# Optimization experiments

Hardware: AMD Instinct MI355X
Metric: run time of the kernel (lower is better)

The kernel has to match this reference:

```python
import jax, jax.numpy as jnp
import numpy as np

DIM = 256
NUM_HEADS = 4
HEAD_DIM = DIM // NUM_HEADS
MLP_HIDDEN = int(DIM * 2.0)
SCALE = HEAD_DIM ** -0.5
LN_EPS = 1e-5


def _layernorm(x, gamma, beta):
    mu = jnp.mean(x, axis=-1, keepdims=True)
    var = jnp.mean(jnp.square(x - mu), axis=-1, keepdims=True)
    return (x - mu) * jax.lax.rsqrt(var + LN_EPS) * gamma + beta


def setup_inputs() -> dict:
    key = jax.random.key(0)
    ks = jax.random.split(key, 8)
    B, C, N, P = 8, DIM, 64, 256
    s = 0.02
    return {
        "x": jax.random.normal(ks[0], (B, C, N, P), dtype=jnp.float32),
        # torch Linear weights stored [out_features, in_features]
        "W_qkv": jax.random.normal(ks[1], (3 * DIM, DIM), dtype=jnp.float32) * s,
        "W_proj": jax.random.normal(ks[2], (DIM, DIM), dtype=jnp.float32) * s,
        "b_proj": jnp.zeros((DIM,), dtype=jnp.float32),
        "ln1_g": jnp.ones((DIM,), dtype=jnp.float32),
        "ln1_b": jnp.zeros((DIM,), dtype=jnp.float32),
        "ln2_g": jnp.ones((DIM,), dtype=jnp.float32),
        "ln2_b": jnp.zeros((DIM,), dtype=jnp.float32),
        "W_mlp1": jax.random.normal(ks[3], (MLP_HIDDEN, DIM), dtype=jnp.float32) * s,
        "b_mlp1": jnp.zeros((MLP_HIDDEN,), dtype=jnp.float32),
        "W_mlp2": jax.random.normal(ks[4], (DIM, MLP_HIDDEN), dtype=jnp.float32) * s,
        "b_mlp2": jnp.zeros((DIM,), dtype=jnp.float32),
    }


def reference(x, W_qkv, W_proj, b_proj, ln1_g, ln1_b, ln2_g, ln2_b,
              W_mlp1, b_mlp1, W_mlp2, b_mlp2):
    B, C, N, P = x.shape
    H, D = NUM_HEADS, HEAD_DIM
    # [B,C,N,P] -> [B*N, P, C]
    x_seq = jnp.transpose(x, (0, 2, 3, 1)).reshape(B * N, P, C)
    shortcut = x_seq

    h = _layernorm(x_seq, ln1_g, ln1_b)
    qkv = jnp.einsum('spc,oc->spo', h, W_qkv)              # [BN, P, 3C]
    qkv = qkv.reshape(B * N, P, 3, H, D)
    q = jnp.transpose(qkv[:, :, 0], (0, 2, 1, 3))          # [BN, H, P, D]
    k = jnp.transpose(qkv[:, :, 1], (0, 2, 1, 3))
    v = jnp.transpose(qkv[:, :, 2], (0, 2, 1, 3))

    attn = jnp.einsum('shpd,shqd->shpq', q, k) * SCALE     # [BN, H, P, P]
    attn = jax.nn.softmax(attn, axis=-1)
    o = jnp.einsum('shpq,shqd->shpd', attn, v)             # [BN, H, P, D]
    o = jnp.transpose(o, (0, 2, 1, 3)).reshape(B * N, P, C)
    o = jnp.einsum('spc,oc->spo', o, W_proj) + b_proj

    x_seq = shortcut + o

    h2 = _layernorm(x_seq, ln2_g, ln2_b)
    m = jnp.einsum('spc,oc->spo', h2, W_mlp1) + b_mlp1
    m = jax.nn.gelu(m, approximate=False)
    m = jnp.einsum('sph,oh->spo', m, W_mlp2) + b_mlp2
    x_seq = x_seq + m

    out = x_seq.reshape(B, N, P, C)
    return jnp.transpose(out, (0, 3, 1, 2))                # [B, C, N, P]
```

## Files before the change

### kernel.cpp

```cpp
#include <hip/hip_runtime.h>
#include <stdint.h>
#include <math.h>


#define DEV static __device__ __forceinline__

typedef __bf16 bf16x8 __attribute__((ext_vector_type(8)));
typedef float  f32x4  __attribute__((ext_vector_type(4)));

union B8 { bf16x8 v; uint4 q; uint32_t u[4]; uint16_t h[8]; };

DEV uint16_t f2bf(float f) {
  uint32_t u = __float_as_uint(f);
  return (uint16_t)((u + 0x7FFFu + ((u >> 16) & 1u)) >> 16);
}
DEV float bf2f(uint16_t h) { return __uint_as_float(((uint32_t)h) << 16); }
DEV uint32_t pk2(float a, float b) { return (uint32_t)f2bf(a) | ((uint32_t)f2bf(b) << 16); }

DEV f32x4 mfma16(const B8& a, const B8& b, f32x4 c) {
  return __builtin_amdgcn_mfma_f32_16x16x32_bf16(a.v, b.v, c, 0, 0, 0);
}

DEV uint32_t shfl_u(uint32_t v, int src) { return (uint32_t)__shfl((int)v, src, 64); }

DEV B8 mk(const uint32_t* w) {
  B8 x; x.u[0] = w[0]; x.u[1] = w[1]; x.u[2] = w[2]; x.u[3] = w[3]; return x;
}

DEV void xpose(const uint32_t* pk0, const uint32_t* pk1, int kd, int g, int r, uint32_t* out) {
  const int sA = 32 * (g & 1) + r;
  const int sB = sA + 16;
  const int tA = 2 * kd, tB = 2 * kd + 1;
  uint32_t a0 = shfl_u(pk0[tA], sA), b0 = shfl_u(pk0[tB], sA);
  uint32_t a1 = shfl_u(pk1[tA], sA), b1 = shfl_u(pk1[tB], sA);
  uint32_t a2 = shfl_u(pk0[tA], sB), b2 = shfl_u(pk0[tB], sB);
  uint32_t a3 = shfl_u(pk1[tA], sB), b3 = shfl_u(pk1[tB], sB);
  const bool hi = g >= 2;
  out[0] = hi ? b0 : a0;
  out[1] = hi ? b1 : a1;
  out[2] = hi ? b2 : a2;
  out[3] = hi ? b3 : a3;
}

__global__ void transformer_prep(const float* __restrict__ wqkv,
                                 const float* __restrict__ wproj,
                                 const float* __restrict__ w1,
                                 const float* __restrict__ w2,
                                 uint16_t* __restrict__ dst) {
  int e = blockIdx.x * 256 + threadIdx.x;
  const float* src; int C, local;
  if (e < 196608)      { src = wqkv;  C = 256; local = e; }
  else if (e < 262144) { src = wproj; C = 256; local = e - 196608; }
  else if (e < 393216) { src = w1;    C = 256; local = e - 262144; }
  else                 { src = w2;    C = 512; local = e - 393216; }
  int k32 = C >> 5;
  int tile = local >> 9, within = local & 511;
  int ln = within >> 3, j = within & 7;
  int tr = tile / k32, tk = tile - tr * k32;
  int row = tr * 16 + (ln & 15), col = tk * 32 + (ln >> 4) * 8 + j;
  float v = src[row * C + col];
  if (e < 65536) v *= 0.18033688011112042f;
  dst[e] = f2bf(v);
}

__global__ __launch_bounds__(512, 2) void transformer_k1(
    const float* __restrict__ x,
    const float* __restrict__ bproj,
    const float* __restrict__ ln1g, const float* __restrict__ ln1b,
    const uint16_t* __restrict__ wf,
    uint16_t* __restrict__ osc,
    float* __restrict__ out) {
  __shared__ __attribute__((aligned(16))) uint8_t lds[65536];
  const int tid = threadIdx.x;
  const int lane = tid & 63;
  const int wv = tid >> 6;
  const int r = lane & 15;
  const int g = lane >> 4;
  const int s = blockIdx.x;
  const int bb = s >> 6, nn = s & 63;
  const float* xs = x + (size_t)bb * 4194304 + (size_t)nn * 256;
  float* outp = out + (size_t)bb * 4194304 + (size_t)nn * 256;
  const f32x4 fz = {0.f, 0.f, 0.f, 0.f};

  uint32_t hfrag[2][8][4];
  float s1[2] = {0.f, 0.f}, s2[2] = {0.f, 0.f};
#pragma unroll
  for (int rt = 0; rt < 2; ++rt) {
    int p = 32 * wv + 16 * rt + r;
#pragma unroll
    for (int kt = 0; kt < 8; ++kt) {
      int c0 = 32 * kt + 8 * g;
      float v[8];
#pragma unroll
      for (int j = 0; j < 8; ++j) {
        v[j] = xs[(size_t)(c0 + j) * 16384 + p];
        s1[rt] += v[j];
        s2[rt] += v[j] * v[j];
      }
#pragma unroll
      for (int w = 0; w < 4; ++w) hfrag[rt][kt][w] = pk2(v[2 * w], v[2 * w + 1]);
    }
  }
  float mu[2], rs[2];
#pragma unroll
  for (int rt = 0; rt < 2; ++rt) {
    float a = s1[rt]; a += __shfl_xor(a, 16, 64); a += __shfl_xor(a, 32, 64);
    float b = s2[rt]; b += __shfl_xor(b, 16, 64); b += __shfl_xor(b, 32, 64);
    mu[rt] = a * (1.0f / 256.0f);
    float var = b * (1.0f / 256.0f) - mu[rt] * mu[rt];
    rs[rt] = rsqrtf(var + 1e-5f);
  }
#pragma unroll
  for (int kt = 0; kt < 8; ++kt) {
    int c0 = 32 * kt + 8 * g;
    f32x4 gA = *(const f32x4*)(ln1g + c0), gB = *(const f32x4*)(ln1g + c0 + 4);
    f32x4 bA = *(const f32x4*)(ln1b + c0), bB = *(const f32x4*)(ln1b + c0 + 4);
#pragma unroll
    for (int rt = 0; rt < 2; ++rt) {
#pragma unroll
      for (int w = 0; w < 4; ++w) {
        uint32_t pw = hfrag[rt][kt][w];
        float lo = bf2f((uint16_t)(pw & 0xFFFFu));
        float hi = bf2f((uint16_t)(pw >> 16));
        float glo = (w < 2) ? gA[2 * w] : gB[2 * w - 4];
        float ghi = (w < 2) ? gA[2 * w + 1] : gB[2 * w - 3];
        float blo = (w < 2) ? bA[2 * w] : bB[2 * w - 4];
        float bhi = (w < 2) ? bA[2 * w + 1] : bB[2 * w - 3];
        lo = (lo - mu[rt]) * rs[rt] * glo + blo;
        hi = (hi - mu[rt]) * rs[rt] * ghi + bhi;
        hfrag[rt][kt][w] = pk2(lo, hi);
      }
    }
  }

#pragma unroll 1
  for (int hd = 0; hd < 4; ++hd) {
#pragma unroll
    for (int m = 0; m < 2; ++m) {
      f32x4 acc[2][4];
#pragma unroll
      for (int rt = 0; rt < 2; ++rt)
#pragma unroll
        for (int ct = 0; ct < 4; ++ct) acc[rt][ct] = fz;
#pragma unroll
      for (int kt = 0; kt < 8; ++kt) {
#pragma unroll
        for (int ct = 0; ct < 4; ++ct) {
          B8 wfr;
          wfr.q = *(const uint4*)(wf + (size_t)((((m + 1) * 16 + hd * 4 + ct) * 8 + kt) * 512) + lane * 8);
#pragma unroll
          for (int rt = 0; rt < 2; ++rt) {
            B8 a = mk(hfrag[rt][kt]);
            acc[rt][ct] = mfma16(a, wfr, acc[rt][ct]);
          }
        }
      }
#pragma unroll
      for (int rt = 0; rt < 2; ++rt) {
#pragma unroll
        for (int ct = 0; ct < 4; ++ct) {
          int d = 16 * ct + r;
          int q0 = 32 * wv + 16 * rt + 4 * g;
          if (m == 0) {
#pragma unroll
            for (int i = 0; i < 4; ++i) {
              int qq = q0 + i;
              *(uint16_t*)(lds + ((qq * 128 + d * 2) ^ ((qq & 7) << 4))) = f2bf(acc[rt][ct][i]);
            }
          } else {
            uint2 pv;
            pv.x = pk2(acc[rt][ct][0], acc[rt][ct][1]);
            pv.y = pk2(acc[rt][ct][2], acc[rt][ct][3]);
            *(uint2*)(lds + ((32768 + d * 512 + q0 * 2) ^ ((d & 7) << 4))) = pv;
          }
        }
      }
    }
    __syncthreads();

#pragma unroll 1
    for (int pt = 0; pt < 2; ++pt) {
      f32x4 qT[4];
#pragma unroll
      for (int mt = 0; mt < 4; ++mt) qT[mt] = fz;
#pragma unroll
      for (int kt = 0; kt < 8; ++kt) {
        B8 hb = mk(hfrag[pt][kt]);
#pragma unroll
        for (int mt = 0; mt < 4; ++mt) {
          B8 wa;
          wa.q = *(const uint4*)(wf + (size_t)(((hd * 4 + mt) * 8 + kt) * 512) + lane * 8);
          qT[mt] = mfma16(wa, hb, qT[mt]);
        }
      }
      uint32_t pq0[4], pq1[4];
#pragma unroll
      for (int mt = 0; mt < 4; ++mt) {
        pq0[mt] = pk2(qT[mt][0], qT[mt][1]);
        pq1[mt] = pk2(qT[mt][2], qT[mt][3]);
      }
      uint32_t qb[2][4];
#pragma unroll
      for (int kd = 0; kd < 2; ++kd) xpose(pq0, pq1, kd, g, r, qb[kd]);

      float m_ = -1e30f, l_ = 0.f;
      f32x4 oT[4];
#pragma unroll
      for (int dt = 0; dt < 4; ++dt) oT[dt] = fz;

#pragma unroll 1
      for (int chk = 0; chk < 4; ++chk) {
        f32x4 sT[4];
#pragma unroll
        for (int qt = 0; qt < 4; ++qt) sT[qt] = fz;
#pragma unroll
        for (int kd = 0; kd < 2; ++kd) {
          B8 qf = mk(qb[kd]);
#pragma unroll
          for (int qt = 0; qt < 4; ++qt) {
            int qq = chk * 64 + 16 * qt + r;
            B8 ka;
            ka.q = *(const uint4*)(lds + ((qq * 128 + (32 * kd + 8 * g) * 2) ^ ((qq & 7) << 4)));
            sT[qt] = mfma16(ka, qf, sT[qt]);
          }
        }
        float tmax = sT[0][0];
#pragma unroll
        for (int qt = 0; qt < 4; ++qt)
#pragma unroll
          for (int i = 0; i < 4; ++i) tmax = fmaxf(tmax, sT[qt][i]);
        tmax = fmaxf(tmax, __shfl_xor(tmax, 16, 64));
        tmax = fmaxf(tmax, __shfl_xor(tmax, 32, 64));
        float mn = fmaxf(m_, tmax);
        float fcor = exp2f(m_ - mn);
        float ts = 0.f;
#pragma unroll
        for (int qt = 0; qt < 4; ++qt)
#pragma unroll
          for (int i = 0; i < 4; ++i) {
            float e = exp2f(sT[qt][i] - mn);
            sT[qt][i] = e;
            ts += e;
          }
        ts += __shfl_xor(ts, 16, 64);
        ts += __shfl_xor(ts, 32, 64);
        l_ = l_ * fcor + ts;
        m_ = mn;
#pragma unroll
        for (int dt = 0; dt < 4; ++dt)
#pragma unroll
          for (int i = 0; i < 4; ++i) oT[dt][i] *= fcor;
        uint32_t pp0[4], pp1[4];
#pragma unroll
        for (int qt = 0; qt < 4; ++qt) {
          pp0[qt] = pk2(sT[qt][0], sT[qt][1]);
          pp1[qt] = pk2(sT[qt][2], sT[qt][3]);
        }
#pragma unroll
        for (int qk = 0; qk < 2; ++qk) {
          uint32_t pb[4];
          xpose(pp0, pp1, qk, g, r, pb);
          B8 pf = mk(pb);
#pragma unroll
          for (int dt = 0; dt < 4; ++dt) {
            B8 va;
            va.q = *(const uint4*)(lds + ((32768 + (16 * dt + r) * 512 + (chk * 64 + 32 * qk + 8 * g) * 2) ^ ((r & 7) << 4)));
            oT[dt] = mfma16(va, pf, oT[dt]);
          }
        }
      }
      float inv = 1.0f / l_;
      uint32_t po0[4], po1[4];
#pragma unroll
      for (int dt = 0; dt < 4; ++dt) {
        po0[dt] = pk2(oT[dt][0] * inv, oT[dt][1] * inv);
        po1[dt] = pk2(oT[dt][2] * inv, oT[dt][3] * inv);
      }
#pragma unroll
      for (int kd = 0; kd < 2; ++kd) {
        uint32_t ofr[4];
        xpose(po0, po1, kd, g, r, ofr);
        B8 t; t.u[0] = ofr[0]; t.u[1] = ofr[1]; t.u[2] = ofr[2]; t.u[3] = ofr[3];
        *(uint4*)(osc + (size_t)((s * 16 + 2 * wv + pt) * 8 + 2 * hd + kd) * 512 + lane * 8) = t.q;
      }
    }
    __syncthreads();
  }

#pragma unroll 1
  for (int q3 = 0; q3 < 4; ++q3) {
    f32x4 acc[2][4];
#pragma unroll
    for (int rt = 0; rt < 2; ++rt)
#pragma unroll
      for (int ct = 0; ct < 4; ++ct) acc[rt][ct] = fz;
#pragma unroll
    for (int kt = 0; kt < 8; ++kt) {
      B8 a[2];
#pragma unroll
      for (int rt = 0; rt < 2; ++rt)
        a[rt].q = *(const uint4*)(osc + (size_t)((s * 16 + 2 * wv + rt) * 8 + kt) * 512 + lane * 8);
#pragma unroll
      for (int ct = 0; ct < 4; ++ct) {
        B8 wfr;
        wfr.q = *(const uint4*)(wf + 196608 + (size_t)(((q3 * 4 + ct) * 8 + kt) * 512) + lane * 8);
#pragma unroll
        for (int rt = 0; rt < 2; ++rt) acc[rt][ct] = mfma16(a[rt], wfr, acc[rt][ct]);
      }
    }
#pragma unroll
    for (int rt = 0; rt < 2; ++rt) {
#pragma unroll
      for (int ct = 0; ct < 4; ++ct) {
        int c = q3 * 64 + 16 * ct + r;
        float bias = bproj[c];
        int p0 = 32 * wv + 16 * rt + 4 * g;
        f32x4 res = *(const f32x4*)(xs + (size_t)c * 16384 + p0);
        f32x4 x2v;
#pragma unroll
        for (int i = 0; i < 4; ++i) x2v[i] = acc[rt][ct][i] + bias + res[i];
        *(f32x4*)(outp + (size_t)c * 16384 + p0) = x2v;
      }
    }
  }
}

__global__ __launch_bounds__(512, 2) void transformer_k2(
    const float* __restrict__ ln2g, const float* __restrict__ ln2b,
    const uint16_t* __restrict__ w1f, const uint16_t* __restrict__ w2f,
    const float* __restrict__ bm1, const float* __restrict__ bm2,
    float* __restrict__ out) {
  __shared__ __attribute__((aligned(16))) uint8_t lds[68608];
  const int tid = threadIdx.x;
  const int lane = tid & 63;
  const int wv = tid >> 6;
  const int r = lane & 15, g = lane >> 4;
  const int bid = blockIdx.x;
  const int s = bid >> 2, tg = bid & 3;
  const int bb = s >> 6, nn = s & 63;
  float* outp = out + (size_t)bb * 4194304 + (size_t)nn * 256;
  const int tokbase = tg * 64;
  const f32x4 fz = {0.f, 0.f, 0.f, 0.f};
  const int mtw = wv & 3, kth = wv >> 2;
  const int p = tokbase + 16 * mtw + r;

  float v[4][8];
  float s1 = 0.f, s2 = 0.f;
#pragma unroll
  for (int k2l = 0; k2l < 4; ++k2l) {
    int c0 = (kth * 4 + k2l) * 32 + 8 * g;
#pragma unroll
    for (int j = 0; j < 8; ++j) {
      float t = outp[(size_t)(c0 + j) * 16384 + p];
      v[k2l][j] = t;
      s1 += t;
      s2 += t * t;
    }
  }
  s1 += __shfl_xor(s1, 16, 64); s1 += __shfl_xor(s1, 32, 64);
  s2 += __shfl_xor(s2, 16, 64); s2 += __shfl_xor(s2, 32, 64);
  if (g == 0) {
    float2 pr; pr.x = s1; pr.y = s2;
    *(float2*)(lds + 65536 + ((16 * mtw + r) * 2 + kth) * 8) = pr;
  }
  __syncthreads();
  if (tid < 64) {
    float2 a = *(const float2*)(lds + 65536 + (tid * 2 + 0) * 8);
    float2 b = *(const float2*)(lds + 65536 + (tid * 2 + 1) * 8);
    float su = a.x + b.x, sq = a.y + b.y;
    float m = su * (1.0f / 256.0f);
    float var = sq * (1.0f / 256.0f) - m * m;
    float2 st; st.x = m; st.y = rsqrtf(var + 1e-5f);
    *(float2*)(lds + 66560 + tid * 8) = st;
  }
  __syncthreads();
  float2 st = *(const float2*)(lds + 66560 + (16 * mtw + r) * 8);
#pragma unroll
  for (int k2l = 0; k2l < 4; ++k2l) {
    int kt = kth * 4 + k2l;
    int c0 = kt * 32 + 8 * g;
    f32x4 gA = *(const f32x4*)(ln2g + c0), gB = *(const f32x4*)(ln2g + c0 + 4);
    f32x4 bA = *(const f32x4*)(ln2b + c0), bB = *(const f32x4*)(ln2b + c0 + 4);
    float nv[8];
#pragma unroll
    for (int j = 0; j < 8; ++j) {
      float gg = (j < 4) ? gA[j] : gB[j - 4];
      float bb2 = (j < 4) ? bA[j] : bB[j - 4];
      nv[j] = (v[k2l][j] - st.x) * st.y * gg + bb2;
    }
    B8 t;
#pragma unroll
    for (int w = 0; w < 4; ++w) t.u[w] = pk2(nv[2 * w], nv[2 * w + 1]);
    *(uint4*)(lds + (mtw * 8 + kt) * 1024 + lane * 16) = t.q;
  }
  __syncthreads();

  f32x4 acc2[4][2];
#pragma unroll
  for (int mt = 0; mt < 4; ++mt)
#pragma unroll
    for (int nt = 0; nt < 2; ++nt) acc2[mt][nt] = fz;

#pragma unroll 1
  for (int half = 0; half < 2; ++half) {
    f32x4 acc1[4][2];
#pragma unroll
    for (int mt = 0; mt < 4; ++mt)
#pragma unroll
      for (int nt = 0; nt < 2; ++nt) acc1[mt][nt] = fz;
#pragma unroll
    for (int kt = 0; kt < 8; ++kt) {
      B8 a[4];
#pragma unroll
      for (int mt = 0; mt < 4; ++mt)
        a[mt].q = *(const uint4*)(lds + (mt * 8 + kt) * 1024 + lane * 16);
#pragma unroll
      for (int nt = 0; nt < 2; ++nt) {
        B8 bfr;
        bfr.q = *(const uint4*)(w1f + (size_t)((((half * 16 + wv * 2 + nt) * 8) + kt) * 512) + lane * 8);
#pragma unroll
        for (int mt = 0; mt < 4; ++mt) acc1[mt][nt] = mfma16(a[mt], bfr, acc1[mt][nt]);
      }
    }
    if (half) __syncthreads();
#pragma unroll
    for (int nt = 0; nt < 2; ++nt) {
      int nl = wv * 32 + 16 * nt + r;
      float bias = bm1[half * 256 + nl];
#pragma unroll
      for (int mt = 0; mt < 4; ++mt) {
#pragma unroll
        for (int i = 0; i < 4; ++i) {
          float vv = acc1[mt][nt][i] + bias;
          vv = 0.5f * vv * (1.0f + erff(vv * 0.70710678118654752440f));
          int lp = (4 * g + i) + 16 * ((nl >> 3) & 3);
          *(uint16_t*)(lds + 32768 + (mt * 8 + wv) * 1024 + lp * 16 + (nl & 7) * 2) = f2bf(vv);
        }
      }
    }
    __syncthreads();
#pragma unroll
    for (int kt = 0; kt < 8; ++kt) {
      B8 a[4];
#pragma unroll
      for (int mt = 0; mt < 4; ++mt)
        a[mt].q = *(const uint4*)(lds + 32768 + (mt * 8 + kt) * 1024 + lane * 16);
#pragma unroll
      for (int nt = 0; nt < 2; ++nt) {
        B8 bfr;
        bfr.q = *(const uint4*)(w2f + (size_t)(((wv * 2 + nt) * 16 + half * 8 + kt) * 512) + lane * 8);
#pragma unroll
        for (int mt = 0; mt < 4; ++mt) acc2[mt][nt] = mfma16(a[mt], bfr, acc2[mt][nt]);
      }
    }
  }

#pragma unroll
  for (int nt = 0; nt < 2; ++nt) {
    int c = wv * 32 + 16 * nt + r;
    float bias = bm2[c];
#pragma unroll
    for (int mt = 0; mt < 4; ++mt) {
      int p0 = tokbase + 16 * mt + 4 * g;
      f32x4 res = *(const f32x4*)(outp + (size_t)c * 16384 + p0);
      f32x4 o;
#pragma unroll
      for (int i = 0; i < 4; ++i) o[i] = res[i] + acc2[mt][nt][i] + bias;
      *(f32x4*)(outp + (size_t)c * 16384 + p0) = o;
    }
  }
}

extern "C" void kernel_launch(void* const* d_in, const int* in_sizes, int n_in,
                              void* d_out, int out_size, void* d_ws, size_t ws_size,
                              hipStream_t stream) {
  (void)in_sizes; (void)n_in; (void)out_size; (void)ws_size;
  const float* x     = (const float*)d_in[0];
  const float* wqkv  = (const float*)d_in[1];
  const float* wproj = (const float*)d_in[2];
  const float* bproj = (const float*)d_in[3];
  const float* ln1g  = (const float*)d_in[4];
  const float* ln1b  = (const float*)d_in[5];
  const float* ln2g  = (const float*)d_in[6];
  const float* ln2b  = (const float*)d_in[7];
  const float* w1    = (const float*)d_in[8];
  const float* bm1   = (const float*)d_in[9];
  const float* w2    = (const float*)d_in[10];
  const float* bm2   = (const float*)d_in[11];
  uint16_t* wbf = (uint16_t*)d_ws;
  uint16_t* osc = wbf + 524288;
  float* out = (float*)d_out;

  transformer_prep<<<2048, 256, 0, stream>>>(wqkv, wproj, w1, w2, wbf);
  transformer_k1<<<512, 512, 0, stream>>>(x, bproj, ln1g, ln1b, wbf, osc, out);
  transformer_k2<<<2048, 512, 0, stream>>>(ln2g, ln2b, wbf + 262144, wbf + 393216, bm1, bm2, out);
}
```

Measured before the change: 730.7 us.

## Double block size to 1024 threads, one 16-token tile per wave

Both fused kernels go from 512 to 1024 threads per block. In the attention kernel each wave now handles one 16-token row tile instead of two. In the MLP kernel each wave computes a slice of the full 512-wide hidden layer in a single pass, with a larger LDS buffer replacing the two-half loop, and LayerNorm2 statistics are reduced across waves through LDS. The aim is more resident waves per CU and better latency hiding from less per-wave work. The cost is that each wave reuses fewer weight fragments, and the larger LDS footprint plus 1024-thread blocks may limit occupancy.

```diff
diff --git a/kernel.cpp b/kernel.cpp
--- a/kernel.cpp
+++ b/kernel.cpp
@@ -63,7 +63,7 @@
   dst[e] = f2bf(v);
 }
 
-__global__ __launch_bounds__(512, 2) void transformer_k1(
+__global__ __launch_bounds__(1024, 4) void transformer_k1(
     const float* __restrict__ x,
     const float* __restrict__ bproj,
     const float* __restrict__ ln1g, const float* __restrict__ ln1b,
@@ -73,7 +73,7 @@
   __shared__ __attribute__((aligned(16))) uint8_t lds[65536];
   const int tid = threadIdx.x;
   const int lane = tid & 63;
-  const int wv = tid >> 6;
+  const int w = tid >> 6;
   const int r = lane & 15;
   const int g = lane >> 4;
   const int s = blockIdx.x;
@@ -82,11 +82,10 @@
   float* outp = out + (size_t)bb * 4194304 + (size_t)nn * 256;
   const f32x4 fz = {0.f, 0.f, 0.f, 0.f};
 
-  uint32_t hfrag[2][8][4];
-  float s1[2] = {0.f, 0.f}, s2[2] = {0.f, 0.f};
-#pragma unroll
-  for (int rt = 0; rt < 2; ++rt) {
-    int p = 32 * wv + 16 * rt + r;
+  uint32_t hfrag[8][4];
+  {
+    float s1 = 0.f, s2 = 0.f;
+    const int p = 16 * w + r;
 #pragma unroll
     for (int kt = 0; kt < 8; ++kt) {
       int c0 = 32 * kt + 8 * g;
@@ -94,41 +93,34 @@
 #pragma unroll
       for (int j = 0; j < 8; ++j) {
         v[j] = xs[(size_t)(c0 + j) * 16384 + p];
-        s1[rt] += v[j];
-        s2[rt] += v[j] * v[j];
-      }
-#pragma unroll
-      for (int w = 0; w < 4; ++w) hfrag[rt][kt][w] = pk2(v[2 * w], v[2 * w + 1]);
-    }
-  }
-  float mu[2], rs[2];
-#pragma unroll
-  for (int rt = 0; rt < 2; ++rt) {
-    float a = s1[rt]; a += __shfl_xor(a, 16, 64); a += __shfl_xor(a, 32, 64);
-    float b = s2[rt]; b += __shfl_xor(b, 16, 64); b += __shfl_xor(b, 32, 64);
-    mu[rt] = a * (1.0f / 256.0f);
-    float var = b * (1.0f / 256.0f) - mu[rt] * mu[rt];
-    rs[rt] = rsqrtf(var + 1e-5f);
-  }
-#pragma unroll
-  for (int kt = 0; kt < 8; ++kt) {
-    int c0 = 32 * kt + 8 * g;
-    f32x4 gA = *(const f32x4*)(ln1g + c0), gB = *(const f32x4*)(ln1g + c0 + 4);
-    f32x4 bA = *(const f32x4*)(ln1b + c0), bB = *(const f32x4*)(ln1b + c0 + 4);
-#pragma unroll
-    for (int rt = 0; rt < 2; ++rt) {
-#pragma unroll
-      for (int w = 0; w < 4; ++w) {
-        uint32_t pw = hfrag[rt][kt][w];
+        s1 += v[j];
+        s2 += v[j] * v[j];
+      }
+#pragma unroll
+      for (int q = 0; q < 4; ++q) hfrag[kt][q] = pk2(v[2 * q], v[2 * q + 1]);
+    }
+    s1 += __shfl_xor(s1, 16, 64); s1 += __shfl_xor(s1, 32, 64);
+    s2 += __shfl_xor(s2, 16, 64); s2 += __shfl_xor(s2, 32, 64);
+    float mu = s1 * (1.0f / 256.0f);
+    float var = s2 * (1.0f / 256.0f) - mu * mu;
+    float rs = rsqrtf(var + 1e-5f);
+#pragma unroll
+    for (int kt = 0; kt < 8; ++kt) {
+      int c0 = 32 * kt + 8 * g;
+      f32x4 gA = *(const f32x4*)(ln1g + c0), gB = *(const f32x4*)(ln1g + c0 + 4);
+      f32x4 bA = *(const f32x4*)(ln1b + c0), bB = *(const f32x4*)(ln1b + c0 + 4);
+#pragma unroll
+      for (int q = 0; q < 4; ++q) {
+        uint32_t pw = hfrag[kt][q];
         float lo = bf2f((uint16_t)(pw & 0xFFFFu));
         float hi = bf2f((uint16_t)(pw >> 16));
-        float glo = (w < 2) ? gA[2 * w] : gB[2 * w - 4];
-        float ghi = (w < 2) ? gA[2 * w + 1] : gB[2 * w - 3];
-        float blo = (w < 2) ? bA[2 * w] : bB[2 * w - 4];
-        float bhi = (w < 2) ? bA[2 * w + 1] : bB[2 * w - 3];
-        lo = (lo - mu[rt]) * rs[rt] * glo + blo;
-        hi = (hi - mu[rt]) * rs[rt] * ghi + bhi;
-        hfrag[rt][kt][w] = pk2(lo, hi);
+        float glo = (q < 2) ? gA[2 * q] : gB[2 * q - 4];
+        float ghi = (q < 2) ? gA[2 * q + 1] : gB[2 * q - 3];
+        float blo = (q < 2) ? bA[2 * q] : bB[2 * q - 4];
+        float bhi = (q < 2) ? bA[2 * q + 1] : bB[2 * q - 3];
+        lo = (lo - mu) * rs * glo + blo;
+        hi = (hi - mu) * rs * ghi + bhi;
+        hfrag[kt][q] = pk2(lo, hi);
       }
     }
   }
@@ -137,55 +129,46 @@
   for (int hd = 0; hd < 4; ++hd) {
 #pragma unroll
     for (int m = 0; m < 2; ++m) {
-      f32x4 acc[2][4];
-#pragma unroll
-      for (int rt = 0; rt < 2; ++rt)
-#pragma unroll
-        for (int ct = 0; ct < 4; ++ct) acc[rt][ct] = fz;
+      f32x4 acc[4];
+#pragma unroll
+      for (int ct = 0; ct < 4; ++ct) acc[ct] = fz;
 #pragma unroll
       for (int kt = 0; kt < 8; ++kt) {
+        B8 a = mk(hfrag[kt]);
 #pragma unroll
         for (int ct = 0; ct < 4; ++ct) {
           B8 wfr;
           wfr.q = *(const uint4*)(wf + (size_t)((((m + 1) * 16 + hd * 4 + ct) * 8 + kt) * 512) + lane * 8);
-#pragma unroll
-          for (int rt = 0; rt < 2; ++rt) {
-            B8 a = mk(hfrag[rt][kt]);
-            acc[rt][ct] = mfma16(a, wfr, acc[rt][ct]);
+          acc[ct] = mfma16(a, wfr, acc[ct]);
+        }
+      }
+#pragma unroll
+      for (int ct = 0; ct < 4; ++ct) {
+        int d = 16 * ct + r;
+        int q0 = 16 * w + 4 * g;
+        if (m == 0) {
+#pragma unroll
+          for (int i = 0; i < 4; ++i) {
+            int qq = q0 + i;
+            *(uint16_t*)(lds + ((qq * 128 + d * 2) ^ ((qq & 7) << 4))) = f2bf(acc[ct][i]);
           }
-        }
-      }
-#pragma unroll
-      for (int rt = 0; rt < 2; ++rt) {
-#pragma unroll
-        for (int ct = 0; ct < 4; ++ct) {
-          int d = 16 * ct + r;
-          int q0 = 32 * wv + 16 * rt + 4 * g;
-          if (m == 0) {
-#pragma unroll
-            for (int i = 0; i < 4; ++i) {
-              int qq = q0 + i;
-              *(uint16_t*)(lds + ((qq * 128 + d * 2) ^ ((qq & 7) << 4))) = f2bf(acc[rt][ct][i]);
-            }
-          } else {
-            uint2 pv;
-            pv.x = pk2(acc[rt][ct][0], acc[rt][ct][1]);
-            pv.y = pk2(acc[rt][ct][2], acc[rt][ct][3]);
-            *(uint2*)(lds + ((32768 + d * 512 + q0 * 2) ^ ((d & 7) << 4))) = pv;
-          }
+        } else {
+          uint2 pv;
+          pv.x = pk2(acc[ct][0], acc[ct][1]);
+          pv.y = pk2(acc[ct][2], acc[ct][3]);
+          *(uint2*)(lds + ((32768 + d * 512 + q0 * 2) ^ ((d & 7) << 4))) = pv;
         }
       }
     }
     __syncthreads();
 
-#pragma unroll 1
-    for (int pt = 0; pt < 2; ++pt) {
+    {
       f32x4 qT[4];
 #pragma unroll
       for (int mt = 0; mt < 4; ++mt) qT[mt] = fz;
 #pragma unroll
       for (int kt = 0; kt < 8; ++kt) {
-        B8 hb = mk(hfrag[pt][kt]);
+        B8 hb = mk(hfrag[kt]);
 #pragma unroll
         for (int mt = 0; mt < 4; ++mt) {
           B8 wa;
@@ -281,7 +264,7 @@
         uint32_t ofr[4];
         xpose(po0, po1, kd, g, r, ofr);
         B8 t; t.u[0] = ofr[0]; t.u[1] = ofr[1]; t.u[2] = ofr[2]; t.u[3] = ofr[3];
-        *(uint4*)(osc + (size_t)((s * 16 + 2 * wv + pt) * 8 + 2 * hd + kd) * 512 + lane * 8) = t.q;
+        *(uint4*)(osc + (size_t)((s * 16 + w) * 8 + 2 * hd + kd) * 512 + lane * 8) = t.q;
       }
     }
     __syncthreads();
@@ -289,51 +272,43 @@
 
 #pragma unroll 1
   for (int q3 = 0; q3 < 4; ++q3) {
-    f32x4 acc[2][4];
-#pragma unroll
-    for (int rt = 0; rt < 2; ++rt)
-#pragma unroll
-      for (int ct = 0; ct < 4; ++ct) acc[rt][ct] = fz;
+    f32x4 acc[4];
+#pragma unroll
+    for (int ct = 0; ct < 4; ++ct) acc[ct] = fz;
 #pragma unroll
     for (int kt = 0; kt < 8; ++kt) {
-      B8 a[2];
-#pragma unroll
-      for (int rt = 0; rt < 2; ++rt)
-        a[rt].q = *(const uint4*)(osc + (size_t)((s * 16 + 2 * wv + rt) * 8 + kt) * 512 + lane * 8);
+      B8 a;
+      a.q = *(const uint4*)(osc + (size_t)((s * 16 + w) * 8 + kt) * 512 + lane * 8);
 #pragma unroll
       for (int ct = 0; ct < 4; ++ct) {
         B8 wfr;
         wfr.q = *(const uint4*)(wf + 196608 + (size_t)(((q3 * 4 + ct) * 8 + kt) * 512) + lane * 8);
-#pragma unroll
-        for (int rt = 0; rt < 2; ++rt) acc[rt][ct] = mfma16(a[rt], wfr, acc[rt][ct]);
-      }
-    }
-#pragma unroll
-    for (int rt = 0; rt < 2; ++rt) {
-#pragma unroll
-      for (int ct = 0; ct < 4; ++ct) {
-        int c = q3 * 64 + 16 * ct + r;
-        float bias = bproj[c];
-        int p0 = 32 * wv + 16 * rt + 4 * g;
-        f32x4 res = *(const f32x4*)(xs + (size_t)c * 16384 + p0);
-        f32x4 x2v;
-#pragma unroll
-        for (int i = 0; i < 4; ++i) x2v[i] = acc[rt][ct][i] + bias + res[i];
-        *(f32x4*)(outp + (size_t)c * 16384 + p0) = x2v;
-      }
-    }
-  }
-}
-
-__global__ __launch_bounds__(512, 2) void transformer_k2(
+        acc[ct] = mfma16(a, wfr, acc[ct]);
+      }
+    }
+#pragma unroll
+    for (int ct = 0; ct < 4; ++ct) {
+      int c = q3 * 64 + 16 * ct + r;
+      float bias = bproj[c];
+      int p0 = 16 * w + 4 * g;
+      f32x4 res = *(const f32x4*)(xs + (size_t)c * 16384 + p0);
+      f32x4 x2v;
+#pragma unroll
+      for (int i = 0; i < 4; ++i) x2v[i] = acc[ct][i] + bias + res[i];
+      *(f32x4*)(outp + (size_t)c * 16384 + p0) = x2v;
+    }
+  }
+}
+
+__global__ __launch_bounds__(1024, 4) void transformer_k2(
     const float* __restrict__ ln2g, const float* __restrict__ ln2b,
     const uint16_t* __restrict__ w1f, const uint16_t* __restrict__ w2f,
     const float* __restrict__ bm1, const float* __restrict__ bm2,
     float* __restrict__ out) {
-  __shared__ __attribute__((aligned(16))) uint8_t lds[68608];
+  __shared__ __attribute__((aligned(16))) uint8_t lds[106496];
   const int tid = threadIdx.x;
   const int lane = tid & 63;
-  const int wv = tid >> 6;
+  const int w = tid >> 6;
   const int r = lane & 15, g = lane >> 4;
   const int bid = blockIdx.x;
   const int s = bid >> 2, tg = bid & 3;
@@ -341,123 +316,111 @@
   float* outp = out + (size_t)bb * 4194304 + (size_t)nn * 256;
   const int tokbase = tg * 64;
   const f32x4 fz = {0.f, 0.f, 0.f, 0.f};
-  const int mtw = wv & 3, kth = wv >> 2;
-  const int p = tokbase + 16 * mtw + r;
-
-  float v[4][8];
-  float s1 = 0.f, s2 = 0.f;
-#pragma unroll
-  for (int k2l = 0; k2l < 4; ++k2l) {
-    int c0 = (kth * 4 + k2l) * 32 + 8 * g;
-#pragma unroll
-    for (int j = 0; j < 8; ++j) {
-      float t = outp[(size_t)(c0 + j) * 16384 + p];
-      v[k2l][j] = t;
+
+  float v[16];
+  {
+    float s1 = 0.f, s2 = 0.f;
+    const int p = tokbase + lane;
+#pragma unroll
+    for (int j = 0; j < 16; ++j) {
+      float t = outp[(size_t)(w * 16 + j) * 16384 + p];
+      v[j] = t;
       s1 += t;
       s2 += t * t;
     }
-  }
-  s1 += __shfl_xor(s1, 16, 64); s1 += __shfl_xor(s1, 32, 64);
-  s2 += __shfl_xor(s2, 16, 64); s2 += __shfl_xor(s2, 32, 64);
-  if (g == 0) {
     float2 pr; pr.x = s1; pr.y = s2;
-    *(float2*)(lds + 65536 + ((16 * mtw + r) * 2 + kth) * 8) = pr;
+    *(float2*)(lds + 98304 + (w * 64 + lane) * 8) = pr;
   }
   __syncthreads();
-  if (tid < 64) {
-    float2 a = *(const float2*)(lds + 65536 + (tid * 2 + 0) * 8);
-    float2 b = *(const float2*)(lds + 65536 + (tid * 2 + 1) * 8);
-    float su = a.x + b.x, sq = a.y + b.y;
-    float m = su * (1.0f / 256.0f);
-    float var = sq * (1.0f / 256.0f) - m * m;
-    float2 st; st.x = m; st.y = rsqrtf(var + 1e-5f);
-    *(float2*)(lds + 66560 + tid * 8) = st;
+  {
+    float su = 0.f, sq = 0.f;
+#pragma unroll
+    for (int w2 = 0; w2 < 16; ++w2) {
+      float2 pr = *(const float2*)(lds + 98304 + (w2 * 64 + lane) * 8);
+      su += pr.x;
+      sq += pr.y;
+    }
+    float mu = su * (1.0f / 256.0f);
+    float var = sq * (1.0f / 256.0f) - mu * mu;
+    float rs = rsqrtf(var + 1e-5f);
+    uint32_t pk[8];
+#pragma unroll
+    for (int q = 0; q < 4; ++q) {
+      int c0 = w * 16 + q * 4;
+      f32x4 gv = *(const f32x4*)(ln2g + c0);
+      f32x4 bv = *(const f32x4*)(ln2b + c0);
+      float n0 = (v[q * 4 + 0] - mu) * rs * gv[0] + bv[0];
+      float n1 = (v[q * 4 + 1] - mu) * rs * gv[1] + bv[1];
+      float n2 = (v[q * 4 + 2] - mu) * rs * gv[2] + bv[2];
+      float n3 = (v[q * 4 + 3] - mu) * rs * gv[3] + bv[3];
+      pk[q * 2 + 0] = pk2(n0, n1);
+      pk[q * 2 + 1] = pk2(n2, n3);
+    }
+    const int mt = lane >> 4;
+    const int kt = w >> 1;
+#pragma unroll
+    for (int hblk = 0; hblk < 2; ++hblk) {
+      int lanep = (lane & 15) + 32 * (w & 1) + 16 * hblk;
+      uint4 t;
+      t.x = pk[hblk * 4 + 0]; t.y = pk[hblk * 4 + 1];
+      t.z = pk[hblk * 4 + 2]; t.w = pk[hblk * 4 + 3];
+      *(uint4*)(lds + (mt * 8 + kt) * 1024 + lanep * 16) = t;
+    }
   }
   __syncthreads();
-  float2 st = *(const float2*)(lds + 66560 + (16 * mtw + r) * 8);
-#pragma unroll
-  for (int k2l = 0; k2l < 4; ++k2l) {
-    int kt = kth * 4 + k2l;
-    int c0 = kt * 32 + 8 * g;
-    f32x4 gA = *(const f32x4*)(ln2g + c0), gB = *(const f32x4*)(ln2g + c0 + 4);
-    f32x4 bA = *(const f32x4*)(ln2b + c0), bB = *(const f32x4*)(ln2b + c0 + 4);
-    float nv[8];
-#pragma unroll
-    for (int j = 0; j < 8; ++j) {
-      float gg = (j < 4) ? gA[j] : gB[j - 4];
-      float bb2 = (j < 4) ? bA[j] : bB[j - 4];
-      nv[j] = (v[k2l][j] - st.x) * st.y * gg + bb2;
-    }
-    B8 t;
-#pragma unroll
-    for (int w = 0; w < 4; ++w) t.u[w] = pk2(nv[2 * w], nv[2 * w + 1]);
-    *(uint4*)(lds + (mtw * 8 + kt) * 1024 + lane * 16) = t.q;
+
+  f32x4 acc1[4][2];
+#pragma unroll
+  for (int mt = 0; mt < 4; ++mt)
+#pragma unroll
+    for (int nt = 0; nt < 2; ++nt) acc1[mt][nt] = fz;
+#pragma unroll
+  for (int kt = 0; kt < 8; ++kt) {
+    B8 a[4];
+#pragma unroll
+    for (int mt = 0; mt < 4; ++mt)
+      a[mt].q = *(const uint4*)(lds + (mt * 8 + kt) * 1024 + lane * 16);
+#pragma unroll
+    for (int nt = 0; nt < 2; ++nt) {
+      B8 bfr;
+      bfr.q = *(const uint4*)(w1f + (size_t)(((2 * w + nt) * 8 + kt) * 512) + lane * 8);
+#pragma unroll
+      for (int mt = 0; mt < 4; ++mt) acc1[mt][nt] = mfma16(a[mt], bfr, acc1[mt][nt]);
+    }
+  }
+#pragma unroll
+  for (int nt = 0; nt < 2; ++nt) {
+    float bias = bm1[(2 * w + nt) * 16 + r];
+#pragma unroll
+    for (int mt = 0; mt < 4; ++mt) {
+#pragma unroll
+      for (int i = 0; i < 4; ++i) {
+        float vv = acc1[mt][nt][i] + bias;
+        vv = 0.5f * vv * (1.0f + erff(vv * 0.70710678118654752440f));
+        int lanep = (4 * g + i) + 16 * (2 * nt + (r >> 3));
+        *(uint16_t*)(lds + 32768 + (mt * 16 + w) * 1024 + lanep * 16 + (r & 7) * 2) = f2bf(vv);
+      }
+    }
   }
   __syncthreads();
 
-  f32x4 acc2[4][2];
-#pragma unroll
-  for (int mt = 0; mt < 4; ++mt)
-#pragma unroll
-    for (int nt = 0; nt < 2; ++nt) acc2[mt][nt] = fz;
-
-#pragma unroll 1
-  for (int half = 0; half < 2; ++half) {
-    f32x4 acc1[4][2];
-#pragma unroll
-    for (int mt = 0; mt < 4; ++mt)
-#pragma unroll
-      for (int nt = 0; nt < 2; ++nt) acc1[mt][nt] = fz;
-#pragma unroll
-    for (int kt = 0; kt < 8; ++kt) {
-      B8 a[4];
-#pragma unroll
-      for (int mt = 0; mt < 4; ++mt)
-        a[mt].q = *(const uint4*)(lds + (mt * 8 + kt) * 1024 + lane * 16);
-#pragma unroll
-      for (int nt = 0; nt < 2; ++nt) {
-        B8 bfr;
-        bfr.q = *(const uint4*)(w1f + (size_t)((((half * 16 + wv * 2 + nt) * 8) + kt) * 512) + lane * 8);
-#pragma unroll
-        for (int mt = 0; mt < 4; ++mt) acc1[mt][nt] = mfma16(a[mt], bfr, acc1[mt][nt]);
-      }
-    }
-    if (half) __syncthreads();
-#pragma unroll
-    for (int nt = 0; nt < 2; ++nt) {
-      int nl = wv * 32 + 16 * nt + r;
-      float bias = bm1[half * 256 + nl];
-#pragma unroll
-      for (int mt = 0; mt < 4; ++mt) {
-#pragma unroll
-        for (int i = 0; i < 4; ++i) {
-          float vv = acc1[mt][nt][i] + bias;
-          vv = 0.5f * vv * (1.0f + erff(vv * 0.70710678118654752440f));
-          int lp = (4 * g + i) + 16 * ((nl >> 3) & 3);
-          *(uint16_t*)(lds + 32768 + (mt * 8 + wv) * 1024 + lp * 16 + (nl & 7) * 2) = f2bf(vv);
-        }
-      }
-    }
-    __syncthreads();
-#pragma unroll
-    for (int kt = 0; kt < 8; ++kt) {
-      B8 a[4];
-#pragma unroll
-      for (int mt = 0; mt < 4; ++mt)
-        a[mt].q = *(const uint4*)(lds + 32768 + (mt * 8 + kt) * 1024 + lane * 16);
-#pragma unroll
-      for (int nt = 0; nt < 2; ++nt) {
-        B8 bfr;
-        bfr.q = *(const uint4*)(w2f + (size_t)(((wv * 2 + nt) * 16 + half * 8 + kt) * 512) + lane * 8);
-#pragma unroll
-        for (int mt = 0; mt < 4; ++mt) acc2[mt][nt] = mfma16(a[mt], bfr, acc2[mt][nt]);
-      }
-    }
-  }
-
-#pragma unroll
-  for (int nt = 0; nt < 2; ++nt) {
-    int c = wv * 32 + 16 * nt + r;
+  f32x4 acc2[4];
+#pragma unroll
+  for (int mt = 0; mt < 4; ++mt) acc2[mt] = fz;
+#pragma unroll
+  for (int kt = 0; kt < 16; ++kt) {
+    B8 bfr;
+    bfr.q = *(const uint4*)(w2f + (size_t)((w * 16 + kt) * 512) + lane * 8);
+#pragma unroll
+    for (int mt = 0; mt < 4; ++mt) {
+      B8 a;
+      a.q = *(const uint4*)(lds + 32768 + (mt * 16 + kt) * 1024 + lane * 16);
+      acc2[mt] = mfma16(a, bfr, acc2[mt]);
+    }
+  }
+
+  {
+    int c = w * 16 + r;
     float bias = bm2[c];
 #pragma unroll
     for (int mt = 0; mt < 4; ++mt) {
@@ -465,7 +428,7 @@
       f32x4 res = *(const f32x4*)(outp + (size_t)c * 16384 + p0);
       f32x4 o;
 #pragma unroll
-      for (int i = 0; i < 4; ++i) o[i] = res[i] + acc2[mt][nt][i] + bias;
+      for (int i = 0; i < 4; ++i) o[i] = res[i] + acc2[mt][i] + bias;
       *(f32x4*)(outp + (size_t)c * 16384 + p0) = o;
     }
   }
@@ -492,6 +455,6 @@
   float* out = (float*)d_out;
 
   transformer_prep<<<2048, 256, 0, stream>>>(wqkv, wproj, w1, w2, wbf);
-  transformer_k1<<<512, 512, 0, stream>>>(x, bproj, ln1g, ln1b, wbf, osc, out);
-  transformer_k2<<<2048, 512, 0, stream>>>(ln2g, ln2b, wbf + 262144, wbf + 393216, bm1, bm2, out);
-}
+  transformer_k1<<<512, 1024, 0, stream>>>(x, bproj, ln1g, ln1b, wbf, osc, out);
+  transformer_k2<<<2048, 1024, 0, stream>>>(ln2g, ln2b, wbf + 262144, wbf + 393216, bm1, bm2, out);
+}
```

Measured after the change: 710.5 us. -2.8%, faster.
